# Kernel tuning notes

Hardware: AMD Instinct MI355X
Metric: run time of the kernel (lower is better)

Reference implementation:

```python
import jax, jax.numpy as jnp
import numpy as np

VOCAB = 50000
D = 200
N_CONCEPTS = 100000
B = 256
L = 8


def setup_inputs() -> dict:
    key = jax.random.key(0)
    k1, k2, k3 = jax.random.split(key, 3)
    mention_word_ids = jax.random.randint(k1, (B, L), 0, VOCAB)
    word_embedding = jax.random.normal(k2, (VOCAB, D), dtype=jnp.float32)
    dict_embedding = jax.random.normal(k3, (N_CONCEPTS, D), dtype=jnp.float32)
    return {
        "mention_word_ids": mention_word_ids,
        "word_embedding": word_embedding,
        "dict_embedding": dict_embedding,
    }


def reference(mention_word_ids, word_embedding, dict_embedding):
    # Embedding lookup [B, L, D] then mean-pool over tokens (avg_pool2d over L) -> [B, D]
    mention_rep = jnp.mean(word_embedding[mention_word_ids], axis=1)
    # Cosine similarity: dot / (||m|| * ||c||), denominator clamped at 1e-8
    m_norm = jnp.linalg.norm(mention_rep, axis=1, keepdims=True)        # [B, 1]
    c_norm = jnp.linalg.norm(dict_embedding, axis=1, keepdims=True)     # [N, 1]
    denom = jnp.maximum(m_norm * c_norm.T, 1e-8)                        # [B, N]
    sims = jnp.matmul(mention_rep, dict_embedding.T) / denom            # [B, N]
    values = jnp.max(sims, axis=1)
    indices = jnp.argmax(sims, axis=1)
    return values, indices
```

## Files before the change

kernel.cpp:

```cpp
#include <hip/hip_runtime.h>
#include <math.h>

#define BB 256
#define LL 8
#define DD 200
#define NN 100000
#define BN 32
#define NTILE (NN / BN)
#define NGRAN 28
#define GRID_SIM 512
#define NCAND 6

typedef __attribute__((ext_vector_type(8))) __bf16 bf16x8;
typedef __attribute__((ext_vector_type(16))) float f32x16;

__device__ __forceinline__ unsigned f2bf(float x) {
  unsigned u = __float_as_uint(x);
  u = (u + 0x7fffu + ((u >> 16) & 1u)) >> 16;
  return u;
}
__device__ __forceinline__ unsigned pk(float a, float b) {
  return f2bf(a) | (f2bf(b) << 16);
}
__device__ __forceinline__ bool better(float a, int ia, float b, int ib) {
  return (a > b) || (a == b && ia < ib);
}
__device__ __forceinline__ float dot4(float4 f) {
  return f.x * f.x + f.y * f.y + f.z * f.z + f.w * f.w;
}

__global__ __launch_bounds__(256) void prep_kernel(
    const int* __restrict__ ids, const float* __restrict__ we,
    float* __restrict__ repf, unsigned short* __restrict__ abf,
    float* __restrict__ mnorm) {
  int m = blockIdx.x, d = threadIdx.x;
  __shared__ float red[4];
  float r = 0.f;
  if (d < DD) {
    int base = m * LL;
#pragma unroll
    for (int l2 = 0; l2 < LL; ++l2) r += we[(size_t)ids[base + l2] * DD + d];
    r *= 0.125f;
    repf[m * DD + d] = r;
  }
  if (d < NGRAN * 8) {
    int g = d >> 3, wo = d & 7;
    abf[(g * 256 + m) * 8 + wo] = (unsigned short)f2bf(d < DD ? r : 0.f);
  }
  float sq = (d < DD) ? r * r : 0.f;
#pragma unroll
  for (int off = 32; off; off >>= 1) sq += __shfl_down(sq, off);
  if ((threadIdx.x & 63) == 0) red[threadIdx.x >> 6] = sq;
  __syncthreads();
  if (threadIdx.x == 0) mnorm[m] = sqrtf(red[0] + red[1] + red[2] + red[3]);
}

__global__ __launch_bounds__(512, 4) void sim_kernel(
    const float* __restrict__ dict, const uint4* __restrict__ abfT,
    float4* __restrict__ partial) {
  __shared__ uint4 Bs[2][NGRAN * BN];

  int tid = threadIdx.x;
  int w = tid >> 6, l = tid & 63;
  int ln = l & 31, kh = l >> 5;
  int m = w * 32 + ln;

  uint4 areg[14];
#pragma unroll
  for (int j = 0; j < 14; ++j) areg[j] = abfT[(2 * j + kh) * 256 + m];

  int row = tid >> 4, part = tid & 15;
  const bool extra = (part < 2);
  int g0i = part >> 1, h = part & 1;

  if (tid < 192) {
    int buf = tid / 96, u = tid % 96;
    int g = 25 + u / 32, r = u & 31;
    Bs[buf][g * 32 + (r ^ (g & 7))] = make_uint4(0, 0, 0, 0);
  }

  float v1 = -INFINITY, v2 = -INFINITY;
  int i1 = 0x7fffffff, i2 = 0x7fffffff;

  int t0 = blockIdx.x;
  {
    const float* src = dict + (size_t)(t0 * BN + row) * DD;
    float4 f0 = *(const float4*)(src + 4 * part);
    float4 f1 = *(const float4*)(src + 64 + 4 * part);
    float4 f2 = *(const float4*)(src + 128 + 4 * part);
    float4 f3 = extra ? *(const float4*)(src + 192 + 4 * part)
                      : make_float4(0.f, 0.f, 0.f, 0.f);
    float sq = dot4(f0) + dot4(f1) + dot4(f2) + dot4(f3);
    sq += __shfl_xor(sq, 1); sq += __shfl_xor(sq, 2);
    sq += __shfl_xor(sq, 4); sq += __shfl_xor(sq, 8);
    float rs = 1.0f / fmaxf(sqrtf(sq), 1e-8f);
    uint2* B2 = (uint2*)&Bs[0][0];
    B2[(g0i * 32 + (row ^ (g0i & 7))) * 2 + h] =
        make_uint2(pk(f0.x * rs, f0.y * rs), pk(f0.z * rs, f0.w * rs));
    int ga = 8 + g0i;
    B2[(ga * 32 + (row ^ (ga & 7))) * 2 + h] =
        make_uint2(pk(f1.x * rs, f1.y * rs), pk(f1.z * rs, f1.w * rs));
    int gb = 16 + g0i;
    B2[(gb * 32 + (row ^ (gb & 7))) * 2 + h] =
        make_uint2(pk(f2.x * rs, f2.y * rs), pk(f2.z * rs, f2.w * rs));
    if (extra)
      B2[(24 * 32 + (row ^ 0)) * 2 + part] =
          make_uint2(pk(f3.x * rs, f3.y * rs), pk(f3.z * rs, f3.w * rs));
  }
  __syncthreads();

  int cur = 0;
  for (int t = t0; t < NTILE; t += GRID_SIM) {
    bool hn = (t + GRID_SIM) < NTILE;
    float4 f0, f1, f2, f3;
    if (hn) {
      const float* src = dict + (size_t)((t + GRID_SIM) * BN + row) * DD;
      f0 = *(const float4*)(src + 4 * part);
      f1 = *(const float4*)(src + 64 + 4 * part);
      f2 = *(const float4*)(src + 128 + 4 * part);
      f3 = extra ? *(const float4*)(src + 192 + 4 * part)
                 : make_float4(0.f, 0.f, 0.f, 0.f);
    }
    __builtin_amdgcn_sched_barrier(0);

    f32x16 acc;
#pragma unroll
    for (int i = 0; i < 16; ++i) acc[i] = 0.f;
    const uint4* B = Bs[cur];
#pragma unroll
    for (int j = 0; j < 14; ++j) {
      int g = 2 * j + kh;
      bf16x8 a = __builtin_bit_cast(bf16x8, B[g * 32 + (ln ^ (g & 7))]);
      acc = __builtin_amdgcn_mfma_f32_32x32x16_bf16(
          a, __builtin_bit_cast(bf16x8, areg[j]), acc, 0, 0, 0);
    }

    int n0 = t * BN + 4 * kh;
#pragma unroll
    for (int r = 0; r < 16; ++r) {
      int n = n0 + (r & 3) + 8 * (r >> 2);
      float v = acc[r];
      if (v > v1) { v2 = v1; i2 = i1; v1 = v; i1 = n; }
      else if (v > v2) { v2 = v; i2 = n; }
    }

    if (hn) {
      float sq = dot4(f0) + dot4(f1) + dot4(f2) + dot4(f3);
      sq += __shfl_xor(sq, 1); sq += __shfl_xor(sq, 2);
      sq += __shfl_xor(sq, 4); sq += __shfl_xor(sq, 8);
      float rs = 1.0f / fmaxf(sqrtf(sq), 1e-8f);
      uint2* B2 = (uint2*)&Bs[cur ^ 1][0];
      B2[(g0i * 32 + (row ^ (g0i & 7))) * 2 + h] =
          make_uint2(pk(f0.x * rs, f0.y * rs), pk(f0.z * rs, f0.w * rs));
      int ga = 8 + g0i;
      B2[(ga * 32 + (row ^ (ga & 7))) * 2 + h] =
          make_uint2(pk(f1.x * rs, f1.y * rs), pk(f1.z * rs, f1.w * rs));
      int gb = 16 + g0i;
      B2[(gb * 32 + (row ^ (gb & 7))) * 2 + h] =
          make_uint2(pk(f2.x * rs, f2.y * rs), pk(f2.z * rs, f2.w * rs));
      if (extra)
        B2[(24 * 32 + row) * 2 + part] =
            make_uint2(pk(f3.x * rs, f3.y * rs), pk(f3.z * rs, f3.w * rs));
    }
    __syncthreads();
    cur ^= 1;
  }

  float w1 = __shfl_xor(v1, 32); int j1 = __shfl_xor(i1, 32);
  float w2 = __shfl_xor(v2, 32); int j2 = __shfl_xor(i2, 32);
  float o1, o2; int oi1, oi2;
  if (better(w1, j1, v1, i1)) {
    bool tt = better(v1, i1, w2, j2);
    o1 = w1; oi1 = j1; o2 = tt ? v1 : w2; oi2 = tt ? i1 : j2;
  } else {
    bool tt = better(w1, j1, v2, i2);
    o1 = v1; oi1 = i1; o2 = tt ? w1 : v2; oi2 = tt ? j1 : i2;
  }
  if (kh == 0)
    partial[(size_t)m * GRID_SIM + blockIdx.x] =
        make_float4(o1, __int_as_float(oi1), o2, __int_as_float(oi2));
}

__global__ __launch_bounds__(256) void final_kernel(
    const float* __restrict__ dict, const float* __restrict__ repf,
    const float* __restrict__ mnorm, const float4* __restrict__ partial,
    float* __restrict__ out) {
  int m = blockIdx.x, tid = threadIdx.x;
  __shared__ float repL[DD];
  __shared__ int seln[NCAND];
  __shared__ float wv[4]; __shared__ int wi[4];
  __shared__ float finv[NCAND]; __shared__ int finn[NCAND];
  if (tid < DD) repL[tid] = repf[m * DD + tid];
  __syncthreads();

  const float4* pm = partial + (size_t)m * GRID_SIM;
  float cv1[2], cv2[2]; int ci1[2], ci2[2];
#pragma unroll
  for (int e = 0; e < 2; ++e) {
    float4 E = pm[tid + e * 256];
    cv1[e] = E.x; ci1[e] = __float_as_int(E.y);
    cv2[e] = E.z; ci2[e] = __float_as_int(E.w);
  }

  for (int r = 0; r < NCAND; ++r) {
    float bv = -INFINITY; int bi = 0x7fffffff;
#pragma unroll
    for (int e = 0; e < 2; ++e) {
      bool ex1 = false, ex2 = false;
      for (int j = 0; j < r; ++j) {
        int s = seln[j];
        ex1 |= (s == ci1[e]); ex2 |= (s == ci2[e]);
      }
      if (!ex1 && better(cv1[e], ci1[e], bv, bi)) { bv = cv1[e]; bi = ci1[e]; }
      if (!ex2 && better(cv2[e], ci2[e], bv, bi)) { bv = cv2[e]; bi = ci2[e]; }
    }
#pragma unroll
    for (int off = 1; off < 64; off <<= 1) {
      float ov = __shfl_xor(bv, off); int oi = __shfl_xor(bi, off);
      if (better(ov, oi, bv, bi)) { bv = ov; bi = oi; }
    }
    if ((tid & 63) == 0) { wv[tid >> 6] = bv; wi[tid >> 6] = bi; }
    __syncthreads();
    if (tid == 0) {
      float Bv = wv[0]; int Bi = wi[0];
#pragma unroll
      for (int q = 1; q < 4; ++q)
        if (better(wv[q], wi[q], Bv, Bi)) { Bv = wv[q]; Bi = wi[q]; }
      seln[r] = Bi;
    }
    __syncthreads();
  }

  int g = tid >> 5, lane = tid & 31;
  int n = (g < NCAND) ? seln[g] : -1;
  float s1 = 0.f, s2 = 0.f;
  if (n >= 0) {
    for (int d = lane; d < DD; d += 32) {
      float b = dict[(size_t)n * DD + d];
      s1 += repL[d] * b; s2 += b * b;
    }
  }
#pragma unroll
  for (int off = 1; off < 32; off <<= 1) {
    s1 += __shfl_xor(s1, off); s2 += __shfl_xor(s2, off);
  }
  if (lane == 0 && g < NCAND) {
    finv[g] = (n >= 0) ? s1 / fmaxf(mnorm[m] * sqrtf(s2), 1e-8f) : -INFINITY;
    finn[g] = n;
  }
  __syncthreads();
  if (tid == 0) {
    float Bv = finv[0]; int Bi = finn[0];
#pragma unroll
    for (int q = 1; q < NCAND; ++q)
      if (better(finv[q], finn[q], Bv, Bi)) { Bv = finv[q]; Bi = finn[q]; }
    out[m] = Bv;
    out[BB + m] = (float)Bi;
  }
}

extern "C" void kernel_launch(void* const* d_in, const int* in_sizes, int n_in,
                              void* d_out, int out_size, void* d_ws, size_t ws_size,
                              hipStream_t stream) {
  const int* ids = (const int*)d_in[0];
  const float* we = (const float*)d_in[1];
  const float* dict = (const float*)d_in[2];
  float* out = (float*)d_out;

  char* ws = (char*)d_ws;
  unsigned short* abf = (unsigned short*)ws;
  float* repf  = (float*)(ws + 114688);
  float* mnorm = (float*)(ws + 319488);
  float4* partial = (float4*)(ws + 320512);

  prep_kernel<<<BB, 256, 0, stream>>>(ids, we, repf, abf, mnorm);
  sim_kernel<<<GRID_SIM, 512, 0, stream>>>(dict, (const uint4*)abf, partial);
  final_kernel<<<BB, 256, 0, stream>>>(dict, repf, mnorm, partial, out);
}
```

Baseline: 45.67 us.

## Fuse prep, similarity and final kernels into one persistent kernel with atomic grid barriers

Merges the three launches into a single 512-block kernel. The first 256 blocks do the mention embedding prep, all blocks spin on an atomic counter before loading A operands, and the first 256 blocks then wait on a second counter to do the candidate reduction and rescoring. The first dictionary tile load is overlapped with the prep phase. This removes two kernel-launch gaps and their tails, but adds a memset launch and spin-wait barriers that rely on all 512 blocks being co-resident.

```diff
diff --git a/kernel.cpp b/kernel.cpp
--- a/kernel.cpp
+++ b/kernel.cpp
@@ -8,7 +8,7 @@
 #define BN 32
 #define NTILE (NN / BN)
 #define NGRAN 28
-#define GRID_SIM 512
+#define GRIDN 512
 #define NCAND 6
 
 typedef __attribute__((ext_vector_type(8))) __bf16 bf16x8;
@@ -29,45 +29,20 @@
   return f.x * f.x + f.y * f.y + f.z * f.z + f.w * f.w;
 }
 
-__global__ __launch_bounds__(256) void prep_kernel(
+__global__ __launch_bounds__(512, 4) void fused_kernel(
     const int* __restrict__ ids, const float* __restrict__ we,
-    float* __restrict__ repf, unsigned short* __restrict__ abf,
-    float* __restrict__ mnorm) {
-  int m = blockIdx.x, d = threadIdx.x;
-  __shared__ float red[4];
-  float r = 0.f;
-  if (d < DD) {
-    int base = m * LL;
-#pragma unroll
-    for (int l2 = 0; l2 < LL; ++l2) r += we[(size_t)ids[base + l2] * DD + d];
-    r *= 0.125f;
-    repf[m * DD + d] = r;
-  }
-  if (d < NGRAN * 8) {
-    int g = d >> 3, wo = d & 7;
-    abf[(g * 256 + m) * 8 + wo] = (unsigned short)f2bf(d < DD ? r : 0.f);
-  }
-  float sq = (d < DD) ? r * r : 0.f;
-#pragma unroll
-  for (int off = 32; off; off >>= 1) sq += __shfl_down(sq, off);
-  if ((threadIdx.x & 63) == 0) red[threadIdx.x >> 6] = sq;
-  __syncthreads();
-  if (threadIdx.x == 0) mnorm[m] = sqrtf(red[0] + red[1] + red[2] + red[3]);
-}
-
-__global__ __launch_bounds__(512, 4) void sim_kernel(
-    const float* __restrict__ dict, const uint4* __restrict__ abfT,
-    float4* __restrict__ partial) {
+    const float* __restrict__ dict, unsigned short* __restrict__ abf,
+    float* __restrict__ repf, float* __restrict__ mnorm,
+    float4* __restrict__ partial, float* __restrict__ out,
+    int* __restrict__ ctr) {
   __shared__ uint4 Bs[2][NGRAN * BN];
-
-  int tid = threadIdx.x;
-  int w = tid >> 6, l = tid & 63;
-  int ln = l & 31, kh = l >> 5;
-  int m = w * 32 + ln;
-
-  uint4 areg[14];
-#pragma unroll
-  for (int j = 0; j < 14; ++j) areg[j] = abfT[(2 * j + kh) * 256 + m];
+  __shared__ float redA[8];
+  __shared__ float repL[DD];
+  __shared__ float wv[8];  __shared__ int wi[8];
+  __shared__ int seln[NCAND];
+  __shared__ float finv[NCAND]; __shared__ int finn[NCAND];
+
+  const int tid = threadIdx.x;
 
   int row = tid >> 4, part = tid & 15;
   const bool extra = (part < 2);
@@ -79,77 +54,59 @@
     Bs[buf][g * 32 + (r ^ (g & 7))] = make_uint4(0, 0, 0, 0);
   }
 
-  float v1 = -INFINITY, v2 = -INFINITY;
-  int i1 = 0x7fffffff, i2 = 0x7fffffff;
-
-  int t0 = blockIdx.x;
+  if (blockIdx.x < BB) {
+    int mm = blockIdx.x, d = tid;
+    float r = 0.f;
+    if (d < DD) {
+      int base = mm * LL;
+#pragma unroll
+      for (int l2 = 0; l2 < LL; ++l2) r += we[(size_t)ids[base + l2] * DD + d];
+      r *= 0.125f;
+      repf[mm * DD + d] = r;
+    }
+    if (d < NGRAN * 8) {
+      int g = d >> 3, wo = d & 7;
+      abf[(g * 256 + mm) * 8 + wo] = (unsigned short)f2bf(d < DD ? r : 0.f);
+    }
+    float sq = (d < DD) ? r * r : 0.f;
+#pragma unroll
+    for (int off = 32; off; off >>= 1) sq += __shfl_down(sq, off);
+    if ((tid & 63) == 0) redA[tid >> 6] = sq;
+    __syncthreads();
+    if (tid == 0) {
+      float s = 0.f;
+#pragma unroll
+      for (int q = 0; q < 8; ++q) s += redA[q];
+      mnorm[blockIdx.x] = sqrtf(s);
+    }
+    __syncthreads();
+    if (tid == 0)
+      __hip_atomic_fetch_add(&ctr[0], 1, __ATOMIC_RELEASE,
+                             __HIP_MEMORY_SCOPE_AGENT);
+  }
+
   {
-    const float* src = dict + (size_t)(t0 * BN + row) * DD;
-    float4 f0 = *(const float4*)(src + 4 * part);
-    float4 f1 = *(const float4*)(src + 64 + 4 * part);
-    float4 f2 = *(const float4*)(src + 128 + 4 * part);
-    float4 f3 = extra ? *(const float4*)(src + 192 + 4 * part)
-                      : make_float4(0.f, 0.f, 0.f, 0.f);
-    float sq = dot4(f0) + dot4(f1) + dot4(f2) + dot4(f3);
-    sq += __shfl_xor(sq, 1); sq += __shfl_xor(sq, 2);
-    sq += __shfl_xor(sq, 4); sq += __shfl_xor(sq, 8);
-    float rs = 1.0f / fmaxf(sqrtf(sq), 1e-8f);
-    uint2* B2 = (uint2*)&Bs[0][0];
-    B2[(g0i * 32 + (row ^ (g0i & 7))) * 2 + h] =
-        make_uint2(pk(f0.x * rs, f0.y * rs), pk(f0.z * rs, f0.w * rs));
-    int ga = 8 + g0i;
-    B2[(ga * 32 + (row ^ (ga & 7))) * 2 + h] =
-        make_uint2(pk(f1.x * rs, f1.y * rs), pk(f1.z * rs, f1.w * rs));
-    int gb = 16 + g0i;
-    B2[(gb * 32 + (row ^ (gb & 7))) * 2 + h] =
-        make_uint2(pk(f2.x * rs, f2.y * rs), pk(f2.z * rs, f2.w * rs));
-    if (extra)
-      B2[(24 * 32 + (row ^ 0)) * 2 + part] =
-          make_uint2(pk(f3.x * rs, f3.y * rs), pk(f3.z * rs, f3.w * rs));
-  }
-  __syncthreads();
-
-  int cur = 0;
-  for (int t = t0; t < NTILE; t += GRID_SIM) {
-    bool hn = (t + GRID_SIM) < NTILE;
-    float4 f0, f1, f2, f3;
-    if (hn) {
-      const float* src = dict + (size_t)((t + GRID_SIM) * BN + row) * DD;
-      f0 = *(const float4*)(src + 4 * part);
-      f1 = *(const float4*)(src + 64 + 4 * part);
-      f2 = *(const float4*)(src + 128 + 4 * part);
-      f3 = extra ? *(const float4*)(src + 192 + 4 * part)
-                 : make_float4(0.f, 0.f, 0.f, 0.f);
-    }
-    __builtin_amdgcn_sched_barrier(0);
-
-    f32x16 acc;
-#pragma unroll
-    for (int i = 0; i < 16; ++i) acc[i] = 0.f;
-    const uint4* B = Bs[cur];
-#pragma unroll
-    for (int j = 0; j < 14; ++j) {
-      int g = 2 * j + kh;
-      bf16x8 a = __builtin_bit_cast(bf16x8, B[g * 32 + (ln ^ (g & 7))]);
-      acc = __builtin_amdgcn_mfma_f32_32x32x16_bf16(
-          a, __builtin_bit_cast(bf16x8, areg[j]), acc, 0, 0, 0);
-    }
-
-    int n0 = t * BN + 4 * kh;
-#pragma unroll
-    for (int r = 0; r < 16; ++r) {
-      int n = n0 + (r & 3) + 8 * (r >> 2);
-      float v = acc[r];
-      if (v > v1) { v2 = v1; i2 = i1; v1 = v; i1 = n; }
-      else if (v > v2) { v2 = v; i2 = n; }
-    }
-
-    if (hn) {
+    int w = tid >> 6, l = tid & 63;
+    int ln = l & 31, kh = l >> 5;
+    int bm = w * 32 + ln;
+    const uint4* abfT = (const uint4*)abf;
+
+    float v1 = -INFINITY, v2 = -INFINITY;
+    int i1 = 0x7fffffff, i2 = 0x7fffffff;
+
+    int t0 = blockIdx.x;
+    {
+      const float* src = dict + (size_t)(t0 * BN + row) * DD;
+      float4 f0 = *(const float4*)(src + 4 * part);
+      float4 f1 = *(const float4*)(src + 64 + 4 * part);
+      float4 f2 = *(const float4*)(src + 128 + 4 * part);
+      float4 f3 = extra ? *(const float4*)(src + 192 + 4 * part)
+                        : make_float4(0.f, 0.f, 0.f, 0.f);
       float sq = dot4(f0) + dot4(f1) + dot4(f2) + dot4(f3);
       sq += __shfl_xor(sq, 1); sq += __shfl_xor(sq, 2);
       sq += __shfl_xor(sq, 4); sq += __shfl_xor(sq, 8);
       float rs = 1.0f / fmaxf(sqrtf(sq), 1e-8f);
-      uint2* B2 = (uint2*)&Bs[cur ^ 1][0];
+      uint2* B2 = (uint2*)&Bs[0][0];
       B2[(g0i * 32 + (row ^ (g0i & 7))) * 2 + h] =
           make_uint2(pk(f0.x * rs, f0.y * rs), pk(f0.z * rs, f0.w * rs));
       int ga = 8 + g0i;
@@ -162,100 +119,168 @@
         B2[(24 * 32 + row) * 2 + part] =
             make_uint2(pk(f3.x * rs, f3.y * rs), pk(f3.z * rs, f3.w * rs));
     }
-    __syncthreads();
-    cur ^= 1;
+
+    if (tid == 0) {
+      while (__hip_atomic_load(&ctr[0], __ATOMIC_ACQUIRE,
+                               __HIP_MEMORY_SCOPE_AGENT) < BB)
+        __builtin_amdgcn_s_sleep(2);
+    }
+    __syncthreads();
+
+    uint4 areg[14];
+#pragma unroll
+    for (int j = 0; j < 14; ++j) areg[j] = abfT[(2 * j + kh) * 256 + bm];
+
+    int cur = 0;
+    for (int t = t0; t < NTILE; t += GRIDN) {
+      bool hn = (t + GRIDN) < NTILE;
+      float4 f0, f1, f2, f3;
+      if (hn) {
+        const float* src = dict + (size_t)((t + GRIDN) * BN + row) * DD;
+        f0 = *(const float4*)(src + 4 * part);
+        f1 = *(const float4*)(src + 64 + 4 * part);
+        f2 = *(const float4*)(src + 128 + 4 * part);
+        f3 = extra ? *(const float4*)(src + 192 + 4 * part)
+                   : make_float4(0.f, 0.f, 0.f, 0.f);
+      }
+      __builtin_amdgcn_sched_barrier(0);
+
+      f32x16 acc;
+#pragma unroll
+      for (int i = 0; i < 16; ++i) acc[i] = 0.f;
+      const uint4* B = Bs[cur];
+#pragma unroll
+      for (int j = 0; j < 14; ++j) {
+        int g = 2 * j + kh;
+        bf16x8 a = __builtin_bit_cast(bf16x8, B[g * 32 + (ln ^ (g & 7))]);
+        acc = __builtin_amdgcn_mfma_f32_32x32x16_bf16(
+            a, __builtin_bit_cast(bf16x8, areg[j]), acc, 0, 0, 0);
+      }
+
+      int n0 = t * BN + 4 * kh;
+#pragma unroll
+      for (int r = 0; r < 16; ++r) {
+        int n = n0 + (r & 3) + 8 * (r >> 2);
+        float v = acc[r];
+        if (v > v1) { v2 = v1; i2 = i1; v1 = v; i1 = n; }
+        else if (v > v2) { v2 = v; i2 = n; }
+      }
+
+      if (hn) {
+        float sq = dot4(f0) + dot4(f1) + dot4(f2) + dot4(f3);
+        sq += __shfl_xor(sq, 1); sq += __shfl_xor(sq, 2);
+        sq += __shfl_xor(sq, 4); sq += __shfl_xor(sq, 8);
+        float rs = 1.0f / fmaxf(sqrtf(sq), 1e-8f);
+        uint2* B2 = (uint2*)&Bs[cur ^ 1][0];
+        B2[(g0i * 32 + (row ^ (g0i & 7))) * 2 + h] =
+            make_uint2(pk(f0.x * rs, f0.y * rs), pk(f0.z * rs, f0.w * rs));
+        int ga = 8 + g0i;
+        B2[(ga * 32 + (row ^ (ga & 7))) * 2 + h] =
+            make_uint2(pk(f1.x * rs, f1.y * rs), pk(f1.z * rs, f1.w * rs));
+        int gb = 16 + g0i;
+        B2[(gb * 32 + (row ^ (gb & 7))) * 2 + h] =
+            make_uint2(pk(f2.x * rs, f2.y * rs), pk(f2.z * rs, f2.w * rs));
+        if (extra)
+          B2[(24 * 32 + row) * 2 + part] =
+              make_uint2(pk(f3.x * rs, f3.y * rs), pk(f3.z * rs, f3.w * rs));
+      }
+      __syncthreads();
+      cur ^= 1;
+    }
+
+    float w1 = __shfl_xor(v1, 32); int j1 = __shfl_xor(i1, 32);
+    float w2 = __shfl_xor(v2, 32); int j2 = __shfl_xor(i2, 32);
+    float o1, o2; int oi1, oi2;
+    if (better(w1, j1, v1, i1)) {
+      bool tt = better(v1, i1, w2, j2);
+      o1 = w1; oi1 = j1; o2 = tt ? v1 : w2; oi2 = tt ? i1 : j2;
+    } else {
+      bool tt = better(w1, j1, v2, i2);
+      o1 = v1; oi1 = i1; o2 = tt ? w1 : v2; oi2 = tt ? j1 : i2;
+    }
+    if (kh == 0)
+      partial[(size_t)bm * GRIDN + blockIdx.x] =
+          make_float4(o1, __int_as_float(oi1), o2, __int_as_float(oi2));
   }
 
-  float w1 = __shfl_xor(v1, 32); int j1 = __shfl_xor(i1, 32);
-  float w2 = __shfl_xor(v2, 32); int j2 = __shfl_xor(i2, 32);
-  float o1, o2; int oi1, oi2;
-  if (better(w1, j1, v1, i1)) {
-    bool tt = better(v1, i1, w2, j2);
-    o1 = w1; oi1 = j1; o2 = tt ? v1 : w2; oi2 = tt ? i1 : j2;
-  } else {
-    bool tt = better(w1, j1, v2, i2);
-    o1 = v1; oi1 = i1; o2 = tt ? w1 : v2; oi2 = tt ? j1 : i2;
-  }
-  if (kh == 0)
-    partial[(size_t)m * GRID_SIM + blockIdx.x] =
-        make_float4(o1, __int_as_float(oi1), o2, __int_as_float(oi2));
-}
-
-__global__ __launch_bounds__(256) void final_kernel(
-    const float* __restrict__ dict, const float* __restrict__ repf,
-    const float* __restrict__ mnorm, const float4* __restrict__ partial,
-    float* __restrict__ out) {
-  int m = blockIdx.x, tid = threadIdx.x;
-  __shared__ float repL[DD];
-  __shared__ int seln[NCAND];
-  __shared__ float wv[4]; __shared__ int wi[4];
-  __shared__ float finv[NCAND]; __shared__ int finn[NCAND];
-  if (tid < DD) repL[tid] = repf[m * DD + tid];
   __syncthreads();
-
-  const float4* pm = partial + (size_t)m * GRID_SIM;
-  float cv1[2], cv2[2]; int ci1[2], ci2[2];
-#pragma unroll
-  for (int e = 0; e < 2; ++e) {
-    float4 E = pm[tid + e * 256];
-    cv1[e] = E.x; ci1[e] = __float_as_int(E.y);
-    cv2[e] = E.z; ci2[e] = __float_as_int(E.w);
-  }
-
-  for (int r = 0; r < NCAND; ++r) {
-    float bv = -INFINITY; int bi = 0x7fffffff;
-#pragma unroll
-    for (int e = 0; e < 2; ++e) {
+  if (tid == 0)
+    __hip_atomic_fetch_add(&ctr[1], 1, __ATOMIC_RELEASE,
+                           __HIP_MEMORY_SCOPE_AGENT);
+  if (blockIdx.x >= BB) return;
+
+  {
+    int m = blockIdx.x;
+    if (tid == 0) {
+      while (__hip_atomic_load(&ctr[1], __ATOMIC_ACQUIRE,
+                               __HIP_MEMORY_SCOPE_AGENT) < GRIDN)
+        __builtin_amdgcn_s_sleep(2);
+    }
+    __syncthreads();
+
+    if (tid < DD) repL[tid] = repf[m * DD + tid];
+    const float4* pmp = partial + (size_t)m * GRIDN;
+    float cv1 = -INFINITY, cv2 = -INFINITY;
+    int ci1 = 0x7fffffff, ci2 = 0x7fffffff;
+    {
+      float4 E = pmp[tid];
+      cv1 = E.x; ci1 = __float_as_int(E.y);
+      cv2 = E.z; ci2 = __float_as_int(E.w);
+    }
+    __syncthreads();
+
+    for (int r = 0; r < NCAND; ++r) {
+      float bv = -INFINITY; int bi = 0x7fffffff;
       bool ex1 = false, ex2 = false;
       for (int j = 0; j < r; ++j) {
         int s = seln[j];
-        ex1 |= (s == ci1[e]); ex2 |= (s == ci2[e]);
-      }
-      if (!ex1 && better(cv1[e], ci1[e], bv, bi)) { bv = cv1[e]; bi = ci1[e]; }
-      if (!ex2 && better(cv2[e], ci2[e], bv, bi)) { bv = cv2[e]; bi = ci2[e]; }
+        ex1 |= (s == ci1); ex2 |= (s == ci2);
+      }
+      if (!ex1 && better(cv1, ci1, bv, bi)) { bv = cv1; bi = ci1; }
+      if (!ex2 && better(cv2, ci2, bv, bi)) { bv = cv2; bi = ci2; }
+#pragma unroll
+      for (int off = 1; off < 64; off <<= 1) {
+        float ov = __shfl_xor(bv, off); int oi = __shfl_xor(bi, off);
+        if (better(ov, oi, bv, bi)) { bv = ov; bi = oi; }
+      }
+      if ((tid & 63) == 0) { wv[tid >> 6] = bv; wi[tid >> 6] = bi; }
+      __syncthreads();
+      if (tid == 0) {
+        float Bv = wv[0]; int Bi = wi[0];
+#pragma unroll
+        for (int q = 1; q < 8; ++q)
+          if (better(wv[q], wi[q], Bv, Bi)) { Bv = wv[q]; Bi = wi[q]; }
+        seln[r] = Bi;
+      }
+      __syncthreads();
+    }
+
+    int g = tid >> 6, lane = tid & 63;
+    int n = (g < NCAND) ? seln[g] : -1;
+    float s1 = 0.f, s2 = 0.f;
+    if (n >= 0) {
+      for (int d = lane; d < DD; d += 64) {
+        float b = dict[(size_t)n * DD + d];
+        s1 += repL[d] * b; s2 += b * b;
+      }
     }
 #pragma unroll
     for (int off = 1; off < 64; off <<= 1) {
-      float ov = __shfl_xor(bv, off); int oi = __shfl_xor(bi, off);
-      if (better(ov, oi, bv, bi)) { bv = ov; bi = oi; }
-    }
-    if ((tid & 63) == 0) { wv[tid >> 6] = bv; wi[tid >> 6] = bi; }
+      s1 += __shfl_xor(s1, off); s2 += __shfl_xor(s2, off);
+    }
+    if (lane == 0 && g < NCAND) {
+      finv[g] = (n >= 0) ? s1 / fmaxf(mnorm[m] * sqrtf(s2), 1e-8f) : -INFINITY;
+      finn[g] = n;
+    }
     __syncthreads();
     if (tid == 0) {
-      float Bv = wv[0]; int Bi = wi[0];
-#pragma unroll
-      for (int q = 1; q < 4; ++q)
-        if (better(wv[q], wi[q], Bv, Bi)) { Bv = wv[q]; Bi = wi[q]; }
-      seln[r] = Bi;
-    }
-    __syncthreads();
-  }
-
-  int g = tid >> 5, lane = tid & 31;
-  int n = (g < NCAND) ? seln[g] : -1;
-  float s1 = 0.f, s2 = 0.f;
-  if (n >= 0) {
-    for (int d = lane; d < DD; d += 32) {
-      float b = dict[(size_t)n * DD + d];
-      s1 += repL[d] * b; s2 += b * b;
-    }
-  }
-#pragma unroll
-  for (int off = 1; off < 32; off <<= 1) {
-    s1 += __shfl_xor(s1, off); s2 += __shfl_xor(s2, off);
-  }
-  if (lane == 0 && g < NCAND) {
-    finv[g] = (n >= 0) ? s1 / fmaxf(mnorm[m] * sqrtf(s2), 1e-8f) : -INFINITY;
-    finn[g] = n;
-  }
-  __syncthreads();
-  if (tid == 0) {
-    float Bv = finv[0]; int Bi = finn[0];
-#pragma unroll
-    for (int q = 1; q < NCAND; ++q)
-      if (better(finv[q], finn[q], Bv, Bi)) { Bv = finv[q]; Bi = finn[q]; }
-    out[m] = Bv;
-    out[BB + m] = (float)Bi;
+      float Bv = finv[0]; int Bi = finn[0];
+#pragma unroll
+      for (int q = 1; q < NCAND; ++q)
+        if (better(finv[q], finn[q], Bv, Bi)) { Bv = finv[q]; Bi = finn[q]; }
+      out[m] = Bv;
+      out[BB + m] = (float)Bi;
+    }
   }
 }
 
@@ -272,8 +297,9 @@
   float* repf  = (float*)(ws + 114688);
   float* mnorm = (float*)(ws + 319488);
   float4* partial = (float4*)(ws + 320512);
-
-  prep_kernel<<<BB, 256, 0, stream>>>(ids, we, repf, abf, mnorm);
-  sim_kernel<<<GRID_SIM, 512, 0, stream>>>(dict, (const uint4*)abf, partial);
-  final_kernel<<<BB, 256, 0, stream>>>(dict, repf, mnorm, partial, out);
-}
+  int* ctr = (int*)(ws + 2417664);
+
+  hipMemsetAsync(ctr, 0, 2 * sizeof(int), stream);
+  fused_kernel<<<GRIDN, 512, 0, stream>>>(ids, we, dict, abf, repf, mnorm,
+                                          partial, out, ctr);
+}
```

Result: slower. 136.6 us (+199.1%).
